# Kernel tuning notes

Hardware: AMD Instinct MI355X
Metric: run time of the kernel (lower is better)

Reference implementation:

```python
import jax, jax.numpy as jnp
import numpy as np

B, N, D = 8, 1024, 1024
H, HD = 16, 64          # n_heads, head_dim = D // H
FF = 2 * D              # SwiGLU hidden dim (ffn_dim_mult=2)
EPS = 1e-5


def setup_inputs() -> dict:
    key = jax.random.key(0)
    ks = jax.random.split(key, 10)
    s = 0.02
    return {
        "x": jax.random.normal(ks[0], (B, N, D), dtype=jnp.float32),
        "attn_norm_scale": jnp.ones((D,), jnp.float32),
        "ffn_norm_scale": jnp.ones((D,), jnp.float32),
        "wq": jax.random.normal(ks[1], (D, D), jnp.float32) * s,
        "bq": jnp.zeros((D,), jnp.float32),
        "wk": jax.random.normal(ks[2], (D, D), jnp.float32) * s,
        "bk": jnp.zeros((D,), jnp.float32),
        "wv": jax.random.normal(ks[3], (D, D), jnp.float32) * s,
        "bv": jnp.zeros((D,), jnp.float32),
        "wo": jax.random.normal(ks[4], (D, D), jnp.float32) * s,
        "bo": jnp.zeros((D,), jnp.float32),
        "w_uv": jax.random.normal(ks[5], (D, 2 * FF), jnp.float32) * s,
        "w_out": jax.random.normal(ks[6], (FF, D), jnp.float32) * s,
    }


def _rmsnorm(x, scale):
    xf = x.astype(jnp.float32)
    y = xf * jax.lax.rsqrt(jnp.mean(xf * xf, axis=-1, keepdims=True) + EPS)
    return scale * y.astype(x.dtype)


def reference(x, attn_norm_scale, ffn_norm_scale, wq, bq, wk, bk, wv, bv,
              wo, bo, w_uv, w_out):
    # FFT2D: fft over channel dim then token dim, keep real part
    x = jnp.fft.fft(jnp.fft.fft(x, axis=-1), axis=-2).real.astype(jnp.float32)

    # --- self attention with pre-RMSNorm and residual ---
    xn = _rmsnorm(x, attn_norm_scale)
    q = (xn @ wq + bq).reshape(B, N, H, HD)
    k = (xn @ wk + bk).reshape(B, N, H, HD)
    v = (xn @ wv + bv).reshape(B, N, H, HD)
    scores = jnp.einsum('bnhd,bmhd->bhnm', q, k) / np.sqrt(HD).astype(np.float32)
    attn = jax.nn.softmax(scores, axis=-1)
    o = jnp.einsum('bhnm,bmhd->bnhd', attn, v).reshape(B, N, D)
    x = (o @ wo + bo) + x

    # --- SwiGLU FFN with pre-RMSNorm and residual ---
    xn = _rmsnorm(x, ffn_norm_scale)
    uv = xn @ w_uv                      # [B, N, 2*FF]
    u, vg = uv[..., :FF], uv[..., FF:]
    x = (jax.nn.silu(u) * vg) @ w_out + x
    return x
```

## Files before the change

kernel.cpp:

```cpp
#include <hip/hip_runtime.h>
#include <stdint.h>

typedef unsigned short u16;
typedef __attribute__((ext_vector_type(8))) __bf16 bf16x8;
typedef __attribute__((ext_vector_type(4))) float f32x4;
typedef __attribute__((ext_vector_type(8))) u16 u16x8;

static __device__ __forceinline__ u16 f2bf(float f){
  uint32_t x = __builtin_bit_cast(uint32_t, f);
  x = (x + 0x7FFFu + ((x >> 16) & 1u)) >> 16;
  return (u16)x;
}
static __device__ __forceinline__ u16 f2bf_fast(float f){
  uint32_t x = __builtin_bit_cast(uint32_t, f);
  return (u16)((x + 0x8000u) >> 16);
}
static __device__ __forceinline__ float bf2f(u16 h){
  uint32_t x = ((uint32_t)h) << 16;
  return __builtin_bit_cast(float, x);
}
static __device__ __forceinline__ f32x4 mfma16(bf16x8 a, bf16x8 b, f32x4 c){
  return __builtin_amdgcn_mfma_f32_16x16x32_bf16(a, b, c, 0, 0, 0);
}
static __device__ __forceinline__ void gload16(const void* g, void* l){
  __builtin_amdgcn_global_load_lds(
      (const __attribute__((address_space(1))) void*)(uintptr_t)g,
      (__attribute__((address_space(3))) void*)(uint32_t)(uintptr_t)l,
      16, 0, 0);
}

__global__ void k_tables(u16* __restrict__ C, u16* __restrict__ S){
  int n = blockIdx.x;
  int m0 = threadIdx.x * 4;
  #pragma unroll
  for (int i = 0; i < 4; ++i){
    int m = m0 + i;
    int ph = (n * m) & 1023;
    float a = (float)ph * (1.0f / 512.0f);
    int idx = n * 1024 + m;
    C[idx] = f2bf(cospif(a)); S[idx] = f2bf(sinpif(a));
  }
}

__global__ void k_tcvt(const float* __restrict__ in, u16* __restrict__ out,
                       int R, int Cc, int64_t inB, int64_t outB){
  __shared__ float t[32][33];
  const float* ip = in + (int64_t)blockIdx.z * inB;
  u16* op = out + (int64_t)blockIdx.z * outB;
  int tc = blockIdx.x * 32, tr = blockIdx.y * 32;
  int lx = threadIdx.x & 31, ly = threadIdx.x >> 5;
  #pragma unroll
  for (int i = 0; i < 32; i += 8)
    t[ly + i][lx] = ip[(int64_t)(tr + ly + i) * Cc + tc + lx];
  __syncthreads();
  #pragma unroll
  for (int i = 0; i < 32; i += 8)
    op[(int64_t)(tc + ly + i) * R + tr + lx] = f2bf(t[lx][ly + i]);
}

__global__ void k_tcvtW(const float* __restrict__ in, u16* __restrict__ out){
  __shared__ float t[32][33];
  int tc = blockIdx.x * 32, tr = blockIdx.y * 32;
  int lx = threadIdx.x & 31, ly = threadIdx.x >> 5;
  #pragma unroll
  for (int i = 0; i < 32; i += 8)
    t[ly + i][lx] = in[(int64_t)(tr + ly + i) * 4096 + tc + lx];
  __syncthreads();
  #pragma unroll
  for (int i = 0; i < 32; i += 8){
    int c = tc + ly + i;
    int pr = (c < 2048) ? ((c >> 4) * 32 + (c & 15))
                        : (((c - 2048) >> 4) * 32 + 16 + ((c - 2048) & 15));
    out[(int64_t)pr * 1024 + tr + lx] = f2bf(t[lx][ly + i]);
  }
}

__global__ void k_bias3(const float* __restrict__ a, const float* __restrict__ b,
                        const float* __restrict__ c, float* __restrict__ o){
  int i = blockIdx.x * 256 + threadIdx.x;
  o[i] = i < 1024 ? a[i] : (i < 2048 ? b[i - 1024] : c[i - 2048]);
}

__global__ __launch_bounds__(256) void k_rmsnorm(const float* __restrict__ x,
                                                 const float* __restrict__ sc,
                                                 u16* __restrict__ out){
  int r = blockIdx.x;
  const float4* px = (const float4*)(x + (int64_t)r * 1024);
  float4 v = px[threadIdx.x];
  float ss = v.x*v.x + v.y*v.y + v.z*v.z + v.w*v.w;
  #pragma unroll
  for (int o = 1; o < 64; o <<= 1) ss += __shfl_xor(ss, o);
  __shared__ float red[4];
  if ((threadIdx.x & 63) == 0) red[threadIdx.x >> 6] = ss;
  __syncthreads();
  float tot = red[0] + red[1] + red[2] + red[3];
  float rs = rsqrtf(tot * (1.0f / 1024.0f) + 1e-5f);
  float4 s4 = ((const float4*)sc)[threadIdx.x];
  ushort4 ov;
  ov.x = f2bf(v.x * rs * s4.x); ov.y = f2bf(v.y * rs * s4.y);
  ov.z = f2bf(v.z * rs * s4.z); ov.w = f2bf(v.w * rs * s4.w);
  ((ushort4*)(out + (int64_t)r * 1024))[threadIdx.x] = ov;
}

__global__ __launch_bounds__(256) void k_fftfin(const u16* __restrict__ Uw,
                                                const float* __restrict__ sc,
                                                float* __restrict__ Y,
                                                u16* __restrict__ xn){
  int row = blockIdx.x;
  int b = row >> 10, k = row & 1023;
  int kp = (k <= 512) ? k : 1024 - k;
  float sgn = (k <= 512) ? -1.0f : 1.0f;
  const u16* ub = Uw + (int64_t)b * (1280 * 1024) + (int64_t)kp * 1024;
  const u16* wb = ub + 640 * 1024;
  int c4 = threadIdx.x * 4;
  ushort4 uu = *(const ushort4*)(ub + c4);
  ushort4 ww = *(const ushort4*)(wb + c4);
  float y0 = bf2f(uu.x) + sgn * bf2f(ww.x);
  float y1 = bf2f(uu.y) + sgn * bf2f(ww.y);
  float y2 = bf2f(uu.z) + sgn * bf2f(ww.z);
  float y3 = bf2f(uu.w) + sgn * bf2f(ww.w);
  float ss = y0*y0 + y1*y1 + y2*y2 + y3*y3;
  #pragma unroll
  for (int o = 1; o < 64; o <<= 1) ss += __shfl_xor(ss, o);
  __shared__ float red[4];
  if ((threadIdx.x & 63) == 0) red[threadIdx.x >> 6] = ss;
  __syncthreads();
  float tot = red[0] + red[1] + red[2] + red[3];
  float rs = rsqrtf(tot * (1.0f / 1024.0f) + 1e-5f);
  float4 s4 = ((const float4*)sc)[threadIdx.x];
  float4 yo; yo.x = y0; yo.y = y1; yo.z = y2; yo.w = y3;
  ((float4*)(Y + (int64_t)row * 1024))[threadIdx.x] = yo;
  ushort4 ov;
  ov.x = f2bf(y0 * rs * s4.x); ov.y = f2bf(y1 * rs * s4.y);
  ov.z = f2bf(y2 * rs * s4.z); ov.w = f2bf(y3 * rs * s4.w);
  ((ushort4*)(xn + (int64_t)row * 1024))[threadIdx.x] = ov;
}

template<bool SILU>
__global__ __launch_bounds__(256, 4) void k_gemm4(
    const u16* __restrict__ A0, const u16* __restrict__ A1,
    const u16* __restrict__ B0, const u16* __restrict__ B1,
    void* Cout, const float* __restrict__ bias, const float* resid,
    int nkt, int rowSplit, int lda, int ldb, int ldc,
    int64_t aB, int64_t bB, int64_t cB, int outBf16)
{
  __shared__ char smem[32768];

  int z = blockIdx.z;
  int nwg = gridDim.x * gridDim.y;
  int bid = blockIdx.y * gridDim.x + blockIdx.x;
  int sw = (bid & 7) * (nwg >> 3) + (bid >> 3);
  int bx = sw % gridDim.x, by = sw / gridDim.x;

  int tm = by * 128, tn = bx * 128;
  int tid = threadIdx.x;
  int lane = tid & 63, w = tid >> 6;
  int lr = lane & 15, lg = lane >> 4;
  int wOffM = (w >> 1) * 64, wOffN = (w & 1) * 64;

  const u16* Ap = ((tm < rowSplit) ? A0 : A1) + (int64_t)z * aB;
  const u16* Bp = ((tm < rowSplit) ? B0 : B1) + (int64_t)z * bB;
  int64_t cOff = (int64_t)z * cB;

  int r0_, kg0_, r1_, kg1_;
  {
    int D = tid * 16, line = D >> 7, sp = ((D >> 4) & 7) ^ (line & 7);
    r0_ = line * 2 + (sp >> 2); kg0_ = sp & 3;
    D = tid * 16 + 4096; line = D >> 7; sp = ((D >> 4) & 7) ^ (line & 7);
    r1_ = line * 2 + (sp >> 2); kg1_ = sp & 3;
  }
  int64_t aAdr0 = (int64_t)(tm + r0_) * lda + kg0_ * 8;
  int64_t aAdr1 = (int64_t)(tm + r1_) * lda + kg1_ * 8;
  int64_t bAdr0 = (int64_t)(tn + r0_) * ldb + kg0_ * 8;
  int64_t bAdr1 = (int64_t)(tn + r1_) * ldb + kg1_ * 8;

  int slotR = (lg + ((lr & 1) << 2)) ^ ((lr >> 1) & 7);
  int aRB = ((wOffM >> 1) + (lr >> 1)) * 128 + slotR * 16;
  int bRB = ((wOffN >> 1) + (lr >> 1)) * 128 + slotR * 16;

  const f32x4 fz = {0.f, 0.f, 0.f, 0.f};
  f32x4 acc[4][4];
  #pragma unroll
  for (int i = 0; i < 4; ++i)
    #pragma unroll
    for (int j = 0; j < 4; ++j) acc[i][j] = fz;

  auto STAGE = [&](int kt, int bf){
    int k0 = kt * 32;
    char* d = smem + bf * 16384 + tid * 16;
    gload16(Ap + aAdr0 + k0, d);
    gload16(Ap + aAdr1 + k0, d + 4096);
    gload16(Bp + bAdr0 + k0, d + 8192);
    gload16(Bp + bAdr1 + k0, d + 12288);
  };

  STAGE(0, 0);
  __syncthreads();
  int buf = 0;
  for (int kt = 0; kt < nkt; ++kt){
    if (kt + 1 < nkt) STAGE(kt + 1, buf ^ 1);
    const char* Ab = smem + buf * 16384;
    const char* Bb = Ab + 8192;
    bf16x8 af[4], bfr[4];
    #pragma unroll
    for (int i = 0; i < 4; ++i) af[i]  = *(const bf16x8*)(Ab + aRB + i * 1024);
    #pragma unroll
    for (int j = 0; j < 4; ++j) bfr[j] = *(const bf16x8*)(Bb + bRB + j * 1024);
    #pragma unroll
    for (int i = 0; i < 4; ++i)
      #pragma unroll
      for (int j = 0; j < 4; ++j)
        acc[i][j] = mfma16(af[i], bfr[j], acc[i][j]);
    __syncthreads();
    buf ^= 1;
  }

  if constexpr (SILU){
    int colBase = ((tn + wOffN) >> 1) + lr;
    #pragma unroll
    for (int i = 0; i < 4; ++i){
      #pragma unroll
      for (int jj = 0; jj < 4; ++jj){
        int row = tm + wOffM + i * 16 + lg * 4 + jj;
        #pragma unroll
        for (int jp = 0; jp < 2; ++jp){
          float u = acc[i][jp * 2][jj], v = acc[i][jp * 2 + 1][jj];
          float s = u / (1.0f + __expf(-u));
          ((u16*)Cout)[(int64_t)row * ldc + colBase + jp * 16] = f2bf(s * v);
        }
      }
    }
  } else {
    #pragma unroll
    for (int i = 0; i < 4; ++i){
      #pragma unroll
      for (int j = 0; j < 4; ++j){
        int col = tn + wOffN + j * 16 + lr;
        float badd = bias ? bias[col] : 0.0f;
        #pragma unroll
        for (int jj = 0; jj < 4; ++jj){
          int row = tm + wOffM + i * 16 + lg * 4 + jj;
          int64_t idx = cOff + (int64_t)row * ldc + col;
          float v = acc[i][j][jj] + badd;
          if (resid) v += resid[idx];
          if (outBf16) ((u16*)Cout)[idx] = f2bf(v);
          else         ((float*)Cout)[idx] = v;
        }
      }
    }
  }
}

__global__ __launch_bounds__(256) void k_vtrans(const u16* __restrict__ qkv,
                                                u16* __restrict__ vt){
  __shared__ u16 T[64 * 65];
  int bh = blockIdx.y; int b = bh >> 4, h = bh & 15;
  int kt = blockIdx.x;
  int t = threadIdx.x;
  const u16* src = qkv + (int64_t)(b * 1024 + kt * 64) * 3072 + 2048 + h * 64;
  #pragma unroll
  for (int i = 0; i < 16; ++i){
    int idx = i * 256 + t;
    int r = idx >> 6, c = idx & 63;
    T[r * 65 + c] = src[(int64_t)r * 3072 + c];
  }
  __syncthreads();
  u16* dst = vt + (int64_t)bh * 65536 + kt * 64;
  #pragma unroll
  for (int i = 0; i < 16; ++i){
    int idx = i * 256 + t;
    int dr = idx >> 6, kc = idx & 63;
    dst[(int64_t)dr * 1024 + kc] = T[kc * 65 + dr];
  }
}

__global__ __launch_bounds__(256, 3) void k_attn2(const u16* __restrict__ qkv,
                                                  const u16* __restrict__ vt,
                                                  u16* __restrict__ O){
  __shared__ u16 Ks[2][4096];
  __shared__ u16 Vts[2][4096];
  __shared__ u16 Pl[4][2304];
  int bh = blockIdx.y; int b = bh >> 4, h = bh & 15;
  int qt = blockIdx.x;
  int t = threadIdx.x, w = t >> 6, lane = t & 63, lr = lane & 15, lg = lane >> 4;
  int sr = t >> 3, sl = t & 7;
  int swz = (sl ^ (sr & 7)) * 8;

  const u16* kg = qkv + (int64_t)b * 1024 * 3072 + 1024 + h * 64;
  const u16* vg = vt + (int64_t)bh * 65536;

  const u16* qrow = qkv + (int64_t)(b * 1024 + qt * 128 + w * 32 + lr) * 3072 + h * 64;
  bf16x8 aq[2][2];
  #pragma unroll
  for (int m = 0; m < 2; ++m)
    #pragma unroll
    for (int kc = 0; kc < 2; ++kc)
      aq[m][kc] = *(const bf16x8*)(qrow + (int64_t)m * 16 * 3072 + kc * 32 + lg * 8);

  const f32x4 fz = {0.f, 0.f, 0.f, 0.f};
  f32x4 o_[2][4];
  float lj[2][4];
  #pragma unroll
  for (int m = 0; m < 2; ++m){
    #pragma unroll
    for (int d = 0; d < 4; ++d) o_[m][d] = fz;
    #pragma unroll
    for (int j = 0; j < 4; ++j) lj[m][j] = 0.f;
  }

  #define STAGE(ktile, bn) do {                                                   \
    int r0 = sr, r1 = 32 + sr;                                                    \
    gload16(kg + (int64_t)((ktile) * 64 + r0) * 3072 + swz,                       \
            (char*)Ks + (bn) * 8192 + (t >> 6) * 1024);                           \
    gload16(kg + (int64_t)((ktile) * 64 + r1) * 3072 + swz,                       \
            (char*)Ks + (bn) * 8192 + 4096 + (t >> 6) * 1024);                    \
    gload16(vg + (int64_t)r0 * 1024 + (ktile) * 64 + swz,                         \
            (char*)Vts + (bn) * 8192 + (t >> 6) * 1024);                          \
    gload16(vg + (int64_t)r1 * 1024 + (ktile) * 64 + swz,                         \
            (char*)Vts + (bn) * 8192 + 4096 + (t >> 6) * 1024);                   \
  } while (0)

  STAGE(0, 0);
  __syncthreads();
  int buf = 0;
  int lsw = lr & 7;

  const float CSC = 0.1803368801111204f;
  const float MSH = 8.656170245333781f;

  #pragma unroll 1
  for (int kt = 0; kt < 16; ++kt){
    if (kt < 15) STAGE(kt + 1, buf ^ 1);

    f32x4 s[2][4];
    #pragma unroll
    for (int m = 0; m < 2; ++m)
      #pragma unroll
      for (int n = 0; n < 4; ++n) s[m][n] = fz;
    #pragma unroll
    for (int n = 0; n < 4; ++n){
      #pragma unroll
      for (int kc = 0; kc < 2; ++kc){
        bf16x8 kb = *(const bf16x8*)&Ks[buf][(n * 16 + lr) * 64 + (((kc * 4 + lg) ^ lsw) * 8)];
        s[0][n] = mfma16(aq[0][kc], kb, s[0][n]);
        s[1][n] = mfma16(aq[1][kc], kb, s[1][n]);
      }
    }

    #pragma unroll
    for (int m = 0; m < 2; ++m){
      #pragma unroll
      for (int j = 0; j < 4; ++j){
        float p0 = exp2f(fmaf(s[m][0][j], CSC, -MSH));
        float p1 = exp2f(fmaf(s[m][1][j], CSC, -MSH));
        float p2 = exp2f(fmaf(s[m][2][j], CSC, -MSH));
        float p3 = exp2f(fmaf(s[m][3][j], CSC, -MSH));
        lj[m][j] += (p0 + p1) + (p2 + p3);
        u16* pb = &Pl[w][(m * 16 + lg * 4 + j) * 72 + lr];
        pb[0]  = f2bf_fast(p0); pb[16] = f2bf_fast(p1);
        pb[32] = f2bf_fast(p2); pb[48] = f2bf_fast(p3);
      }
    }
    asm volatile("s_waitcnt lgkmcnt(0)" ::: "memory");
    __builtin_amdgcn_sched_barrier(0);

    #pragma unroll
    for (int kc = 0; kc < 2; ++kc){
      bf16x8 pa0 = *(const bf16x8*)&Pl[w][(lr) * 72 + kc * 32 + lg * 8];
      bf16x8 pa1 = *(const bf16x8*)&Pl[w][(16 + lr) * 72 + kc * 32 + lg * 8];
      #pragma unroll
      for (int dt = 0; dt < 4; ++dt){
        bf16x8 vb = *(const bf16x8*)&Vts[buf][(dt * 16 + lr) * 64 + (((kc * 4 + lg) ^ lsw) * 8)];
        o_[0][dt] = mfma16(pa0, vb, o_[0][dt]);
        o_[1][dt] = mfma16(pa1, vb, o_[1][dt]);
      }
    }
    __syncthreads();
    buf ^= 1;
  }
  #undef STAGE

  u16* obase = O + (int64_t)(b * 1024 + qt * 128 + w * 32) * 1024 + h * 64;
  #pragma unroll
  for (int m = 0; m < 2; ++m){
    #pragma unroll
    for (int j = 0; j < 4; ++j){
      float l = lj[m][j];
      l += __shfl_xor(l, 1); l += __shfl_xor(l, 2);
      l += __shfl_xor(l, 4); l += __shfl_xor(l, 8);
      float inv = 1.0f / l;
      int q = m * 16 + lg * 4 + j;
      #pragma unroll
      for (int dt = 0; dt < 4; ++dt)
        obase[(int64_t)q * 1024 + dt * 16 + lr] = f2bf(o_[m][dt][j] * inv);
    }
  }
}

extern "C" void kernel_launch(void* const* d_in, const int* in_sizes, int n_in,
                              void* d_out, int out_size, void* d_ws, size_t ws_size,
                              hipStream_t stream)
{
  (void)in_sizes; (void)n_in; (void)out_size; (void)ws_size;
  const float* x    = (const float*)d_in[0];
  const float* ans  = (const float*)d_in[1];
  const float* fns  = (const float*)d_in[2];
  const float* wq   = (const float*)d_in[3];
  const float* bq   = (const float*)d_in[4];
  const float* wk   = (const float*)d_in[5];
  const float* bk   = (const float*)d_in[6];
  const float* wv   = (const float*)d_in[7];
  const float* bvv  = (const float*)d_in[8];
  const float* wo   = (const float*)d_in[9];
  const float* bo   = (const float*)d_in[10];
  const float* wuv  = (const float*)d_in[11];
  const float* wout = (const float*)d_in[12];

  char* ws = (char*)d_ws;
  const size_t MB = 1u << 20;
  const int64_t M1 = 1024 * 1024;
  const int64_t FB = (int64_t)1280 * 1024;
  const int BIG = 1 << 30;
  u16*  xbt   = (u16*)(ws + 0 * MB);
  u16*  Xcs   = (u16*)(ws + 16 * MB);
  u16*  Uw    = (u16*)(ws + 36 * MB);
  u16*  xn    = (u16*)(ws + 56 * MB);
  u16*  qkv   = (u16*)(ws + 0 * MB);
  u16*  vtg   = (u16*)(ws + 72 * MB);
  u16*  Obuf  = (u16*)(ws + 88 * MB);
  u16*  xn2   = (u16*)(ws + 0 * MB);
  u16*  g     = (u16*)(ws + 16 * MB);
  u16*  Cb    = (u16*)(ws + 104 * MB);
  u16*  Sb    = (u16*)(ws + 106 * MB);
  u16*  wqkvt = (u16*)(ws + 108 * MB);
  u16*  wot   = (u16*)(ws + 114 * MB);
  u16*  wuvt  = (u16*)(ws + 116 * MB);
  u16*  woutt = (u16*)(ws + 124 * MB);
  float* bqkv = (float*)(ws + 128 * MB);
  float* outF = (float*)d_out;

  k_tables<<<dim3(1024), 256, 0, stream>>>(Cb, Sb);
  k_tcvt<<<dim3(32, 32, 8), 256, 0, stream>>>(x, xbt, 1024, 1024, M1, M1);
  k_tcvt<<<dim3(32, 32, 1), 256, 0, stream>>>(wq, wqkvt,          1024, 1024, 0, 0);
  k_tcvt<<<dim3(32, 32, 1), 256, 0, stream>>>(wk, wqkvt + M1,     1024, 1024, 0, 0);
  k_tcvt<<<dim3(32, 32, 1), 256, 0, stream>>>(wv, wqkvt + 2 * M1, 1024, 1024, 0, 0);
  k_tcvt<<<dim3(32, 32, 1), 256, 0, stream>>>(wo, wot, 1024, 1024, 0, 0);
  k_tcvtW<<<dim3(128, 32), 256, 0, stream>>>(wuv, wuvt);
  k_tcvt<<<dim3(32, 64, 1), 256, 0, stream>>>(wout, woutt, 2048, 1024, 0, 0);
  k_bias3<<<dim3(12), 256, 0, stream>>>(bq, bk, bvv, bqkv);

  k_gemm4<false><<<dim3(8, 10, 8), 256, 0, stream>>>(
      Cb, Sb - 640 * 1024, xbt, xbt, Xcs, nullptr, nullptr,
      32, 640, 1024, 1024, 1024, 0, M1, FB, 1);
  k_gemm4<false><<<dim3(8, 10, 8), 256, 0, stream>>>(
      Xcs, Xcs, Cb, Sb, Uw, nullptr, nullptr,
      32, 640, 1024, 1024, 1024, FB, 0, FB, 1);
  k_fftfin<<<dim3(8192), 256, 0, stream>>>(Uw, ans, outF, xn);

  k_gemm4<false><<<dim3(24, 64, 1), 256, 0, stream>>>(
      xn, xn, wqkvt, wqkvt, qkv, bqkv, nullptr,
      32, BIG, 1024, 1024, 3072, 0, 0, 0, 1);
  k_vtrans<<<dim3(16, 128), 256, 0, stream>>>(qkv, vtg);
  k_attn2<<<dim3(8, 128), 256, 0, stream>>>(qkv, vtg, Obuf);
  k_gemm4<false><<<dim3(8, 64, 1), 256, 0, stream>>>(
      Obuf, Obuf, wot, wot, d_out, bo, outF,
      32, BIG, 1024, 1024, 1024, 0, 0, 0, 0);

  k_rmsnorm<<<dim3(8192), 256, 0, stream>>>(outF, fns, xn2);
  k_gemm4<true><<<dim3(32, 64, 1), 256, 0, stream>>>(
      xn2, xn2, wuvt, wuvt, g, nullptr, nullptr,
      32, BIG, 1024, 1024, 2048, 0, 0, 0, 1);
  k_gemm4<false><<<dim3(8, 64, 1), 256, 0, stream>>>(
      g, g, woutt, woutt, d_out, nullptr, outF,
      64, BIG, 2048, 2048, 1024, 0, 0, 0, 0);
}
```

Measured before the change: 445.8 us.

## Fuse prep kernels, enlarge attention blocks to 8 waves, unroll GEMM k-loop

Merges the table, transpose/convert and bias preprocessing kernels into a single launch to cut launch overhead. Attention blocks now use 512 threads covering 256 queries, so each staged K/V tile is shared by twice as many waves and each thread issues half the loads. The GEMM main loop is unrolled by two with fixed double buffers and precomputed pointers, which assumes an even number of k-tiles. Fewer resident attention blocks may lower occupancy.

```diff
diff --git a/kernel.cpp b/kernel.cpp
--- a/kernel.cpp
+++ b/kernel.cpp
@@ -29,56 +29,84 @@
       16, 0, 0);
 }
 
-__global__ void k_tables(u16* __restrict__ C, u16* __restrict__ S){
-  int n = blockIdx.x;
-  int m0 = threadIdx.x * 4;
-  #pragma unroll
-  for (int i = 0; i < 4; ++i){
-    int m = m0 + i;
-    int ph = (n * m) & 1023;
-    float a = (float)ph * (1.0f / 512.0f);
-    int idx = n * 1024 + m;
-    C[idx] = f2bf(cospif(a)); S[idx] = f2bf(sinpif(a));
-  }
-}
-
-__global__ void k_tcvt(const float* __restrict__ in, u16* __restrict__ out,
-                       int R, int Cc, int64_t inB, int64_t outB){
-  __shared__ float t[32][33];
-  const float* ip = in + (int64_t)blockIdx.z * inB;
-  u16* op = out + (int64_t)blockIdx.z * outB;
-  int tc = blockIdx.x * 32, tr = blockIdx.y * 32;
-  int lx = threadIdx.x & 31, ly = threadIdx.x >> 5;
+__global__ __launch_bounds__(256) void k_prep(
+    const float* __restrict__ x,  const float* __restrict__ wq,
+    const float* __restrict__ wk, const float* __restrict__ wv,
+    const float* __restrict__ wo, const float* __restrict__ wuv,
+    const float* __restrict__ wout,
+    const float* __restrict__ bq, const float* __restrict__ bk,
+    const float* __restrict__ bv,
+    u16* __restrict__ Cb, u16* __restrict__ Sb, u16* __restrict__ xbt,
+    u16* __restrict__ wqkvt, u16* __restrict__ wot, u16* __restrict__ wuvt,
+    u16* __restrict__ woutt, float* __restrict__ bqkv)
+{
+  int bid = blockIdx.x;
+  int t = threadIdx.x;
+  if (bid < 1024){
+    int n = bid, m0 = t * 4;
+    #pragma unroll
+    for (int i = 0; i < 4; ++i){
+      int m = m0 + i;
+      int ph = (n * m) & 1023;
+      float a = (float)ph * (1.0f / 512.0f);
+      int idx = n * 1024 + m;
+      Cb[idx] = f2bf(cospif(a)); Sb[idx] = f2bf(sinpif(a));
+    }
+    return;
+  }
+  bid -= 1024;
+  if (bid >= 18432){
+    int i = (bid - 18432) * 256 + t;
+    bqkv[i] = i < 1024 ? bq[i] : (i < 2048 ? bk[i - 1024] : bv[i - 2048]);
+    return;
+  }
+  __shared__ float tl[32][33];
+  const float* in; u16* out; int Cc, R, bx, by;
+  int64_t inOff = 0, outOff = 0;
+  bool uvperm = false;
+  if (bid < 8192){
+    int z = bid >> 10, tile = bid & 1023;
+    in = x; out = xbt; Cc = 1024; R = 1024;
+    inOff = (int64_t)z << 20; outOff = (int64_t)z << 20;
+    bx = tile & 31; by = tile >> 5;
+  } else if (bid < 12288){
+    int j = (bid - 8192) >> 10, tile = (bid - 8192) & 1023;
+    const float* srcs[4] = {wq, wk, wv, wo};
+    in = srcs[j]; Cc = 1024; R = 1024;
+    if (j < 3){ out = wqkvt; outOff = (int64_t)j << 20; }
+    else      { out = wot; }
+    bx = tile & 31; by = tile >> 5;
+  } else if (bid < 16384){
+    int tile = bid - 12288;
+    in = wuv; out = wuvt; Cc = 4096; R = 1024; uvperm = true;
+    bx = tile & 127; by = tile >> 7;
+  } else {
+    int tile = bid - 16384;
+    in = wout; out = woutt; Cc = 1024; R = 2048;
+    bx = tile & 31; by = tile >> 6;
+    by = tile >> 5;
+  }
+  int tc = bx * 32, tr = by * 32;
+  int lx = t & 31, ly = t >> 5;
+  const float* ip = in + inOff;
   #pragma unroll
   for (int i = 0; i < 32; i += 8)
-    t[ly + i][lx] = ip[(int64_t)(tr + ly + i) * Cc + tc + lx];
-  __syncthreads();
-  #pragma unroll
-  for (int i = 0; i < 32; i += 8)
-    op[(int64_t)(tc + ly + i) * R + tr + lx] = f2bf(t[lx][ly + i]);
-}
-
-__global__ void k_tcvtW(const float* __restrict__ in, u16* __restrict__ out){
-  __shared__ float t[32][33];
-  int tc = blockIdx.x * 32, tr = blockIdx.y * 32;
-  int lx = threadIdx.x & 31, ly = threadIdx.x >> 5;
-  #pragma unroll
-  for (int i = 0; i < 32; i += 8)
-    t[ly + i][lx] = in[(int64_t)(tr + ly + i) * 4096 + tc + lx];
-  __syncthreads();
-  #pragma unroll
-  for (int i = 0; i < 32; i += 8){
-    int c = tc + ly + i;
-    int pr = (c < 2048) ? ((c >> 4) * 32 + (c & 15))
-                        : (((c - 2048) >> 4) * 32 + 16 + ((c - 2048) & 15));
-    out[(int64_t)pr * 1024 + tr + lx] = f2bf(t[lx][ly + i]);
-  }
-}
-
-__global__ void k_bias3(const float* __restrict__ a, const float* __restrict__ b,
-                        const float* __restrict__ c, float* __restrict__ o){
-  int i = blockIdx.x * 256 + threadIdx.x;
-  o[i] = i < 1024 ? a[i] : (i < 2048 ? b[i - 1024] : c[i - 2048]);
+    tl[ly + i][lx] = ip[(int64_t)(tr + ly + i) * Cc + tc + lx];
+  __syncthreads();
+  if (uvperm){
+    #pragma unroll
+    for (int i = 0; i < 32; i += 8){
+      int c = tc + ly + i;
+      int pr = (c < 2048) ? ((c >> 4) * 32 + (c & 15))
+                          : (((c - 2048) >> 4) * 32 + 16 + ((c - 2048) & 15));
+      out[(int64_t)pr * 1024 + tr + lx] = f2bf(tl[lx][ly + i]);
+    }
+  } else {
+    u16* op = out + outOff;
+    #pragma unroll
+    for (int i = 0; i < 32; i += 8)
+      op[(int64_t)(tc + ly + i) * R + tr + lx] = f2bf(tl[lx][ly + i]);
+  }
 }
 
 __global__ __launch_bounds__(256) void k_rmsnorm(const float* __restrict__ x,
@@ -169,10 +197,10 @@
     D = tid * 16 + 4096; line = D >> 7; sp = ((D >> 4) & 7) ^ (line & 7);
     r1_ = line * 2 + (sp >> 2); kg1_ = sp & 3;
   }
-  int64_t aAdr0 = (int64_t)(tm + r0_) * lda + kg0_ * 8;
-  int64_t aAdr1 = (int64_t)(tm + r1_) * lda + kg1_ * 8;
-  int64_t bAdr0 = (int64_t)(tn + r0_) * ldb + kg0_ * 8;
-  int64_t bAdr1 = (int64_t)(tn + r1_) * ldb + kg1_ * 8;
+  const u16* pA0 = Ap + (int64_t)(tm + r0_) * lda + kg0_ * 8;
+  const u16* pA1 = Ap + (int64_t)(tm + r1_) * lda + kg1_ * 8;
+  const u16* pB0 = Bp + (int64_t)(tn + r0_) * ldb + kg0_ * 8;
+  const u16* pB1 = Bp + (int64_t)(tn + r1_) * ldb + kg1_ * 8;
 
   int slotR = (lg + ((lr & 1) << 2)) ^ ((lr >> 1) & 7);
   int aRB = ((wOffM >> 1) + (lr >> 1)) * 128 + slotR * 16;
@@ -188,18 +216,12 @@
   auto STAGE = [&](int kt, int bf){
     int k0 = kt * 32;
     char* d = smem + bf * 16384 + tid * 16;
-    gload16(Ap + aAdr0 + k0, d);
-    gload16(Ap + aAdr1 + k0, d + 4096);
-    gload16(Bp + bAdr0 + k0, d + 8192);
-    gload16(Bp + bAdr1 + k0, d + 12288);
+    gload16(pA0 + k0, d);
+    gload16(pA1 + k0, d + 4096);
+    gload16(pB0 + k0, d + 8192);
+    gload16(pB1 + k0, d + 12288);
   };
-
-  STAGE(0, 0);
-  __syncthreads();
-  int buf = 0;
-  for (int kt = 0; kt < nkt; ++kt){
-    if (kt + 1 < nkt) STAGE(kt + 1, buf ^ 1);
-    const char* Ab = smem + buf * 16384;
+  auto COMPUTE = [&](const char* Ab){
     const char* Bb = Ab + 8192;
     bf16x8 af[4], bfr[4];
     #pragma unroll
@@ -211,8 +233,17 @@
       #pragma unroll
       for (int j = 0; j < 4; ++j)
         acc[i][j] = mfma16(af[i], bfr[j], acc[i][j]);
+  };
+
+  STAGE(0, 0);
+  __syncthreads();
+  for (int kt = 0; kt < nkt; kt += 2){
+    STAGE(kt + 1, 1);
+    COMPUTE(smem);
     __syncthreads();
-    buf ^= 1;
+    if (kt + 2 < nkt) STAGE(kt + 2, 0);
+    COMPUTE(smem + 16384);
+    __syncthreads();
   }
 
   if constexpr (SILU){
@@ -274,12 +305,12 @@
   }
 }
 
-__global__ __launch_bounds__(256, 3) void k_attn2(const u16* __restrict__ qkv,
+__global__ __launch_bounds__(512, 4) void k_attn2(const u16* __restrict__ qkv,
                                                   const u16* __restrict__ vt,
                                                   u16* __restrict__ O){
   __shared__ u16 Ks[2][4096];
   __shared__ u16 Vts[2][4096];
-  __shared__ u16 Pl[4][2304];
+  __shared__ u16 Pl[8][2304];
   int bh = blockIdx.y; int b = bh >> 4, h = bh & 15;
   int qt = blockIdx.x;
   int t = threadIdx.x, w = t >> 6, lane = t & 63, lr = lane & 15, lg = lane >> 4;
@@ -289,7 +320,7 @@
   const u16* kg = qkv + (int64_t)b * 1024 * 3072 + 1024 + h * 64;
   const u16* vg = vt + (int64_t)bh * 65536;
 
-  const u16* qrow = qkv + (int64_t)(b * 1024 + qt * 128 + w * 32 + lr) * 3072 + h * 64;
+  const u16* qrow = qkv + (int64_t)(b * 1024 + qt * 256 + w * 32 + lr) * 3072 + h * 64;
   bf16x8 aq[2][2];
   #pragma unroll
   for (int m = 0; m < 2; ++m)
@@ -309,15 +340,10 @@
   }
 
   #define STAGE(ktile, bn) do {                                                   \
-    int r0 = sr, r1 = 32 + sr;                                                    \
-    gload16(kg + (int64_t)((ktile) * 64 + r0) * 3072 + swz,                       \
-            (char*)Ks + (bn) * 8192 + (t >> 6) * 1024);                           \
-    gload16(kg + (int64_t)((ktile) * 64 + r1) * 3072 + swz,                       \
-            (char*)Ks + (bn) * 8192 + 4096 + (t >> 6) * 1024);                    \
-    gload16(vg + (int64_t)r0 * 1024 + (ktile) * 64 + swz,                         \
-            (char*)Vts + (bn) * 8192 + (t >> 6) * 1024);                          \
-    gload16(vg + (int64_t)r1 * 1024 + (ktile) * 64 + swz,                         \
-            (char*)Vts + (bn) * 8192 + 4096 + (t >> 6) * 1024);                   \
+    gload16(kg + (int64_t)((ktile) * 64 + sr) * 3072 + swz,                       \
+            (char*)Ks + (bn) * 8192 + t * 16);                                    \
+    gload16(vg + (int64_t)sr * 1024 + (ktile) * 64 + swz,                         \
+            (char*)Vts + (bn) * 8192 + t * 16);                                   \
   } while (0)
 
   STAGE(0, 0);
@@ -380,7 +406,7 @@
   }
   #undef STAGE
 
-  u16* obase = O + (int64_t)(b * 1024 + qt * 128 + w * 32) * 1024 + h * 64;
+  u16* obase = O + (int64_t)(b * 1024 + qt * 256 + w * 32) * 1024 + h * 64;
   #pragma unroll
   for (int m = 0; m < 2; ++m){
     #pragma unroll
@@ -439,15 +465,8 @@
   float* bqkv = (float*)(ws + 128 * MB);
   float* outF = (float*)d_out;
 
-  k_tables<<<dim3(1024), 256, 0, stream>>>(Cb, Sb);
-  k_tcvt<<<dim3(32, 32, 8), 256, 0, stream>>>(x, xbt, 1024, 1024, M1, M1);
-  k_tcvt<<<dim3(32, 32, 1), 256, 0, stream>>>(wq, wqkvt,          1024, 1024, 0, 0);
-  k_tcvt<<<dim3(32, 32, 1), 256, 0, stream>>>(wk, wqkvt + M1,     1024, 1024, 0, 0);
-  k_tcvt<<<dim3(32, 32, 1), 256, 0, stream>>>(wv, wqkvt + 2 * M1, 1024, 1024, 0, 0);
-  k_tcvt<<<dim3(32, 32, 1), 256, 0, stream>>>(wo, wot, 1024, 1024, 0, 0);
-  k_tcvtW<<<dim3(128, 32), 256, 0, stream>>>(wuv, wuvt);
-  k_tcvt<<<dim3(32, 64, 1), 256, 0, stream>>>(wout, woutt, 2048, 1024, 0, 0);
-  k_bias3<<<dim3(12), 256, 0, stream>>>(bq, bk, bvv, bqkv);
+  k_prep<<<dim3(19468), 256, 0, stream>>>(x, wq, wk, wv, wo, wuv, wout,
+      bq, bk, bvv, Cb, Sb, xbt, wqkvt, wot, wuvt, woutt, bqkv);
 
   k_gemm4<false><<<dim3(8, 10, 8), 256, 0, stream>>>(
       Cb, Sb - 640 * 1024, xbt, xbt, Xcs, nullptr, nullptr,
@@ -461,7 +480,7 @@
       xn, xn, wqkvt, wqkvt, qkv, bqkv, nullptr,
       32, BIG, 1024, 1024, 3072, 0, 0, 0, 1);
   k_vtrans<<<dim3(16, 128), 256, 0, stream>>>(qkv, vtg);
-  k_attn2<<<dim3(8, 128), 256, 0, stream>>>(qkv, vtg, Obuf);
+  k_attn2<<<dim3(4, 128), 512, 0, stream>>>(qkv, vtg, Obuf);
   k_gemm4<false><<<dim3(8, 64, 1), 256, 0, stream>>>(
       Obuf, Obuf, wot, wot, d_out, bo, outF,
       32, BIG, 1024, 1024, 1024, 0, 0, 0, 0);
```

Measured after the change: 422.3 us. 5.3% less time.
